# Kernel tuning notes

Measured on AMD Instinct MI355X. Metric: run time of the kernel, lower is better.

The kernel has to match this reference:

```python
import jax, jax.numpy as jnp
import numpy as np


def setup_inputs() -> dict:
    key = jax.random.key(0)
    k1, k2 = jax.random.split(key)
    N, H, W, F = 32, 16, 16, 256
    B, C = 64, 8
    x = jax.random.normal(k1, (N, H, W, F), dtype=jnp.float32)
    # keras 'uniform' initializer: U(-0.05, 0.05)
    T = jax.random.uniform(k2, (F, B, C), dtype=jnp.float32, minval=-0.05, maxval=0.05)
    return {"x": x, "T": T}


def reference(x, T):
    # x: [N,H,W,F], T: [F,B,C]
    M = jnp.einsum('nhwf,fbc->nhwbc', x, T)            # [N,H,W,B,C]
    # all-pairs L1 distance over C between samples i and j
    diff = jnp.abs(M[:, None] - M[None, :])            # [N,N,H,W,B,C]
    norm = jnp.sum(diff, axis=-1)                      # [N,N,H,W,B]
    o_b = jnp.sum(jnp.exp(-norm), axis=1)              # [N,H,W,B]
    return jnp.concatenate([x, o_b], axis=3)           # [N,H,W,F+B]
```

## Files before the change

### kernel.cpp

```cpp
#include <hip/hip_runtime.h>
#include <hip/hip_bf16.h>


namespace {
constexpr int kN = 32;
constexpr int kHW = 256;
constexpr int kF = 256;
constexpr int kB = 64;
constexpr int kOutRow = 320;
constexpr int kMstride = 264;
}

using frag_ab = __attribute__((ext_vector_type(8))) short;
using frag_cd = __attribute__((ext_vector_type(4))) float;

__device__ inline unsigned short f2bf(float f) {
  union { __hip_bfloat16 h; unsigned short u; } c;
  c.h = __float2bfloat16(f);
  return c.u;
}

__device__ inline void unpack8(const uint4& m, float* f) {
  f[0] = __uint_as_float(m.x << 16);  f[1] = __uint_as_float(m.x & 0xffff0000u);
  f[2] = __uint_as_float(m.y << 16);  f[3] = __uint_as_float(m.y & 0xffff0000u);
  f[4] = __uint_as_float(m.z << 16);  f[5] = __uint_as_float(m.z & 0xffff0000u);
  f[6] = __uint_as_float(m.w << 16);  f[7] = __uint_as_float(m.w & 0xffff0000u);
}

__global__ __launch_bounds__(256)
void transpose_T(const float* __restrict__ T, unsigned short* __restrict__ Tt) {
  __shared__ unsigned short tile[64 * 72];
  const int kt = blockIdx.x >> 3;
  const int tt = blockIdx.x & 7;
  const int k0 = kt * 64, t0 = tt * 64;
  const int tid = threadIdx.x;
#pragma unroll
  for (int s = 0; s < 4; ++s) {
    const int r = (tid >> 4) + s * 16;
    const int c = (tid & 15) * 4;
    float4 v = *(const float4*)&T[(size_t)(k0 + r) * 512 + t0 + c];
    tile[(c + 0) * 72 + r] = f2bf(v.x);
    tile[(c + 1) * 72 + r] = f2bf(v.y);
    tile[(c + 2) * 72 + r] = f2bf(v.z);
    tile[(c + 3) * 72 + r] = f2bf(v.w);
  }
  __syncthreads();
#pragma unroll
  for (int s = 0; s < 2; ++s) {
    const int tr = (tid >> 3) + s * 32;
    const int kc = (tid & 7) * 8;
    uint4 o = *(const uint4*)&tile[tr * 72 + kc];
    *(uint4*)&Tt[(size_t)(t0 + tr) * 256 + k0 + kc] = o;
  }
}

__global__ __launch_bounds__(512, 4)
void mbd_main(const float* __restrict__ x, const unsigned short* __restrict__ Tt,
              float* __restrict__ out) {
  __shared__ uint4 Afrag[2 * 8 * 64];
  __shared__ unsigned short Mlds[kN * kMstride];
  const int hw = blockIdx.x & (kHW - 1);
  const int bg = blockIdx.x >> 8;
  const int tid = threadIdx.x;
  const int l = tid & 63, w = tid >> 6;

  const float4* x4 = (const float4*)x;
  float4* out4 = (float4*)out;
#pragma unroll
  for (int s = 0; s < 2; ++s) {
    const int task = tid + s * 512;
    const int n = task >> 5;
    const int k8 = task & 31;
    const size_t xb = (size_t)n * (kHW * kF / 4) + (size_t)hw * (kF / 4) + k8 * 2;
    float4 v0 = x4[xb];
    float4 v1 = x4[xb + 1];
    if ((k8 >> 4) == bg) {
      const size_t ob = (size_t)(n * kHW + hw) * (kOutRow / 4) + k8 * 2;
      out4[ob] = v0;
      out4[ob + 1] = v1;
    }
    uint4 p;
    p.x = (unsigned)f2bf(v0.x) | ((unsigned)f2bf(v0.y) << 16);
    p.y = (unsigned)f2bf(v0.z) | ((unsigned)f2bf(v0.w) << 16);
    p.z = (unsigned)f2bf(v1.x) | ((unsigned)f2bf(v1.y) << 16);
    p.w = (unsigned)f2bf(v1.z) | ((unsigned)f2bf(v1.w) << 16);
    const int rt = n >> 4, kt = k8 >> 2, ln = (n & 15) | ((k8 & 3) << 4);
    Afrag[(rt * 8 + kt) * 64 + ln] = p;
  }
  __syncthreads();

  frag_cd acc[2][2] = {};
#pragma unroll
  for (int kt = 0; kt < 8; ++kt) {
    uint4 a0 = Afrag[(0 * 8 + kt) * 64 + l];
    uint4 a1 = Afrag[(1 * 8 + kt) * 64 + l];
    const int krow = kt * 32 + (l >> 4) * 8;
#pragma unroll
    for (int q = 0; q < 2; ++q) {
      const int tcol = bg * 256 + (w * 2 + q) * 16 + (l & 15);
      uint4 b = *(const uint4*)&Tt[(size_t)tcol * 256 + krow];
      frag_ab af0 = __builtin_bit_cast(frag_ab, a0);
      frag_ab af1 = __builtin_bit_cast(frag_ab, a1);
      frag_ab bf = __builtin_bit_cast(frag_ab, b);
      acc[q][0] = __builtin_amdgcn_mfma_f32_16x16x32_bf16(af0, bf, acc[q][0], 0, 0, 0);
      acc[q][1] = __builtin_amdgcn_mfma_f32_16x16x32_bf16(af1, bf, acc[q][1], 0, 0, 0);
    }
  }

#pragma unroll
  for (int q = 0; q < 2; ++q)
#pragma unroll
    for (int rt = 0; rt < 2; ++rt)
#pragma unroll
      for (int r = 0; r < 4; ++r) {
        const int n = rt * 16 + (l >> 4) * 4 + r;
        const int t = (w * 2 + q) * 16 + (l & 15);
        Mlds[n * kMstride + t] = f2bf(acc[q][rt][r]);
      }
  __syncthreads();

  const int b = tid >> 4;
  const int i0 = (tid & 15) * 2;
  float mi[2][8];
#pragma unroll
  for (int ii = 0; ii < 2; ++ii) {
    uint4 m = *(const uint4*)&Mlds[(i0 + ii) * kMstride + b * 8];
    unpack8(m, mi[ii]);
  }
  float ob0 = 0.f, ob1 = 0.f;
#pragma unroll 4
  for (int j = 0; j < kN; ++j) {
    uint4 m = *(const uint4*)&Mlds[j * kMstride + b * 8];
    float mj[8];
    unpack8(m, mj);
    float n0 = 0.f, n1 = 0.f;
#pragma unroll
    for (int c = 0; c < 8; ++c) {
      n0 += fabsf(mi[0][c] - mj[c]);
      n1 += fabsf(mi[1][c] - mj[c]);
    }
    ob0 += __expf(-n0);
    ob1 += __expf(-n1);
  }
  const int bglob = kF + bg * 32 + b;
  out[(size_t)(i0 * kHW + hw) * kOutRow + bglob] = ob0;
  out[(size_t)((i0 + 1) * kHW + hw) * kOutRow + bglob] = ob1;
}

extern "C" void kernel_launch(void* const* d_in, const int* in_sizes, int n_in,
                              void* d_out, int out_size, void* d_ws, size_t ws_size,
                              hipStream_t stream) {
  const float* x = (const float*)d_in[0];
  const float* T = (const float*)d_in[1];
  float* out = (float*)d_out;
  unsigned short* Tt = (unsigned short*)d_ws;
  (void)in_sizes; (void)n_in; (void)out_size; (void)ws_size;
  transpose_T<<<dim3(32), dim3(256), 0, stream>>>(T, Tt);
  mbd_main<<<dim3(2 * kHW), dim3(512), 0, stream>>>(x, Tt, out);
}
```

Measured before the change: 80.05 us.

## Process all B per block, prepack T into MFMA fragments, coalesce o_b stores

Result: slower. 82.52 us (+3.1%).

```diff
diff --git a/kernel.cpp b/kernel.cpp
--- a/kernel.cpp
+++ b/kernel.cpp
@@ -6,9 +6,8 @@
 constexpr int kN = 32;
 constexpr int kHW = 256;
 constexpr int kF = 256;
-constexpr int kB = 64;
 constexpr int kOutRow = 320;
-constexpr int kMstride = 264;
+constexpr int kMstride = 520;
 }
 
 using frag_ab = __attribute__((ext_vector_type(8))) short;
@@ -28,39 +27,30 @@
 }
 
 __global__ __launch_bounds__(256)
-void transpose_T(const float* __restrict__ T, unsigned short* __restrict__ Tt) {
-  __shared__ unsigned short tile[64 * 72];
-  const int kt = blockIdx.x >> 3;
-  const int tt = blockIdx.x & 7;
-  const int k0 = kt * 64, t0 = tt * 64;
-  const int tid = threadIdx.x;
+void pack_T(const float* __restrict__ T, uint4* __restrict__ Tf) {
+  const int g = blockIdx.x * 256 + threadIdx.x;
+  const int l = g & 63;
+  const int frag = g >> 6;
+  const int tt = frag >> 3, kt = frag & 7;
+  const int col = tt * 16 + (l & 15);
+  const int k0 = kt * 32 + (l >> 4) * 8;
+  unsigned p[4];
 #pragma unroll
-  for (int s = 0; s < 4; ++s) {
-    const int r = (tid >> 4) + s * 16;
-    const int c = (tid & 15) * 4;
-    float4 v = *(const float4*)&T[(size_t)(k0 + r) * 512 + t0 + c];
-    tile[(c + 0) * 72 + r] = f2bf(v.x);
-    tile[(c + 1) * 72 + r] = f2bf(v.y);
-    tile[(c + 2) * 72 + r] = f2bf(v.z);
-    tile[(c + 3) * 72 + r] = f2bf(v.w);
+  for (int jj = 0; jj < 4; ++jj) {
+    float a = T[(size_t)(k0 + jj * 2) * 512 + col];
+    float b = T[(size_t)(k0 + jj * 2 + 1) * 512 + col];
+    p[jj] = (unsigned)f2bf(a) | ((unsigned)f2bf(b) << 16);
   }
-  __syncthreads();
-#pragma unroll
-  for (int s = 0; s < 2; ++s) {
-    const int tr = (tid >> 3) + s * 32;
-    const int kc = (tid & 7) * 8;
-    uint4 o = *(const uint4*)&tile[tr * 72 + kc];
-    *(uint4*)&Tt[(size_t)(t0 + tr) * 256 + k0 + kc] = o;
-  }
+  Tf[g] = make_uint4(p[0], p[1], p[2], p[3]);
 }
 
-__global__ __launch_bounds__(512, 4)
-void mbd_main(const float* __restrict__ x, const unsigned short* __restrict__ Tt,
+__global__ __launch_bounds__(512, 2)
+void mbd_main(const float* __restrict__ x, const uint4* __restrict__ Tf,
               float* __restrict__ out) {
   __shared__ uint4 Afrag[2 * 8 * 64];
-  __shared__ unsigned short Mlds[kN * kMstride];
-  const int hw = blockIdx.x & (kHW - 1);
-  const int bg = blockIdx.x >> 8;
+  __shared__ __align__(16) unsigned short Mlds[kN * kMstride];
+  float* obuf = (float*)Afrag;
+  const int hw = blockIdx.x;
   const int tid = threadIdx.x;
   const int l = tid & 63, w = tid >> 6;
 
@@ -74,11 +64,9 @@
     const size_t xb = (size_t)n * (kHW * kF / 4) + (size_t)hw * (kF / 4) + k8 * 2;
     float4 v0 = x4[xb];
     float4 v1 = x4[xb + 1];
-    if ((k8 >> 4) == bg) {
-      const size_t ob = (size_t)(n * kHW + hw) * (kOutRow / 4) + k8 * 2;
-      out4[ob] = v0;
-      out4[ob + 1] = v1;
-    }
+    const size_t ob = (size_t)(n * kHW + hw) * (kOutRow / 4) + k8 * 2;
+    out4[ob] = v0;
+    out4[ob + 1] = v1;
     uint4 p;
     p.x = (unsigned)f2bf(v0.x) | ((unsigned)f2bf(v0.y) << 16);
     p.y = (unsigned)f2bf(v0.z) | ((unsigned)f2bf(v0.w) << 16);
@@ -89,62 +77,75 @@
   }
   __syncthreads();
 
-  frag_cd acc[2][2] = {};
+  frag_cd acc[4][2] = {};
 #pragma unroll
   for (int kt = 0; kt < 8; ++kt) {
     uint4 a0 = Afrag[(0 * 8 + kt) * 64 + l];
     uint4 a1 = Afrag[(1 * 8 + kt) * 64 + l];
-    const int krow = kt * 32 + (l >> 4) * 8;
+    frag_ab af0 = __builtin_bit_cast(frag_ab, a0);
+    frag_ab af1 = __builtin_bit_cast(frag_ab, a1);
 #pragma unroll
-    for (int q = 0; q < 2; ++q) {
-      const int tcol = bg * 256 + (w * 2 + q) * 16 + (l & 15);
-      uint4 b = *(const uint4*)&Tt[(size_t)tcol * 256 + krow];
-      frag_ab af0 = __builtin_bit_cast(frag_ab, a0);
-      frag_ab af1 = __builtin_bit_cast(frag_ab, a1);
+    for (int q = 0; q < 4; ++q) {
+      const int tT = w * 4 + q;
+      uint4 b = Tf[(tT * 8 + kt) * 64 + l];
       frag_ab bf = __builtin_bit_cast(frag_ab, b);
       acc[q][0] = __builtin_amdgcn_mfma_f32_16x16x32_bf16(af0, bf, acc[q][0], 0, 0, 0);
       acc[q][1] = __builtin_amdgcn_mfma_f32_16x16x32_bf16(af1, bf, acc[q][1], 0, 0, 0);
     }
   }
+  __syncthreads();
 
 #pragma unroll
-  for (int q = 0; q < 2; ++q)
+  for (int q = 0; q < 4; ++q)
 #pragma unroll
     for (int rt = 0; rt < 2; ++rt)
 #pragma unroll
       for (int r = 0; r < 4; ++r) {
         const int n = rt * 16 + (l >> 4) * 4 + r;
-        const int t = (w * 2 + q) * 16 + (l & 15);
+        const int t = (w * 4 + q) * 16 + (l & 15);
         Mlds[n * kMstride + t] = f2bf(acc[q][rt][r]);
       }
   __syncthreads();
 
-  const int b = tid >> 4;
+  const int bA = tid >> 4;
   const int i0 = (tid & 15) * 2;
-  float mi[2][8];
+  float mi[2][2][8];
 #pragma unroll
-  for (int ii = 0; ii < 2; ++ii) {
-    uint4 m = *(const uint4*)&Mlds[(i0 + ii) * kMstride + b * 8];
-    unpack8(m, mi[ii]);
-  }
-  float ob0 = 0.f, ob1 = 0.f;
+  for (int bs = 0; bs < 2; ++bs)
+#pragma unroll
+    for (int ii = 0; ii < 2; ++ii) {
+      uint4 m = *(const uint4*)&Mlds[(i0 + ii) * kMstride + (bA + bs * 32) * 8];
+      unpack8(m, mi[bs][ii]);
+    }
+  float ob[2][2] = {};
 #pragma unroll 4
   for (int j = 0; j < kN; ++j) {
-    uint4 m = *(const uint4*)&Mlds[j * kMstride + b * 8];
-    float mj[8];
-    unpack8(m, mj);
-    float n0 = 0.f, n1 = 0.f;
 #pragma unroll
-    for (int c = 0; c < 8; ++c) {
-      n0 += fabsf(mi[0][c] - mj[c]);
-      n1 += fabsf(mi[1][c] - mj[c]);
+    for (int bs = 0; bs < 2; ++bs) {
+      uint4 m = *(const uint4*)&Mlds[j * kMstride + (bA + bs * 32) * 8];
+      float mj[8];
+      unpack8(m, mj);
+#pragma unroll
+      for (int ii = 0; ii < 2; ++ii) {
+        float nrm = 0.f;
+#pragma unroll
+        for (int c = 0; c < 8; ++c) nrm += fabsf(mi[bs][ii][c] - mj[c]);
+        ob[bs][ii] += __expf(-nrm);
+      }
     }
-    ob0 += __expf(-n0);
-    ob1 += __expf(-n1);
   }
-  const int bglob = kF + bg * 32 + b;
-  out[(size_t)(i0 * kHW + hw) * kOutRow + bglob] = ob0;
-  out[(size_t)((i0 + 1) * kHW + hw) * kOutRow + bglob] = ob1;
+#pragma unroll
+  for (int bs = 0; bs < 2; ++bs)
+#pragma unroll
+    for (int ii = 0; ii < 2; ++ii)
+      obuf[(i0 + ii) * 68 + bA + bs * 32] = ob[bs][ii];
+  __syncthreads();
+  {
+    const int n = tid >> 4;
+    const int b4 = tid & 15;
+    float4 v = *(const float4*)&obuf[n * 68 + b4 * 4];
+    out4[(size_t)(n * kHW + hw) * (kOutRow / 4) + (kF / 4) + b4] = v;
+  }
 }
 
 extern "C" void kernel_launch(void* const* d_in, const int* in_sizes, int n_in,
@@ -153,8 +154,8 @@
   const float* x = (const float*)d_in[0];
   const float* T = (const float*)d_in[1];
   float* out = (float*)d_out;
-  unsigned short* Tt = (unsigned short*)d_ws;
+  uint4* Tf = (uint4*)d_ws;
   (void)in_sizes; (void)n_in; (void)out_size; (void)ws_size;
-  transpose_T<<<dim3(32), dim3(256), 0, stream>>>(T, Tt);
-  mbd_main<<<dim3(2 * kHW), dim3(512), 0, stream>>>(x, Tt, out);
+  pack_T<<<dim3(64), dim3(256), 0, stream>>>(T, Tf);
+  mbd_main<<<dim3(kHW), dim3(512), 0, stream>>>(x, Tf, out);
 }
```
